# Optimization experiments

Measured on AMD Instinct MI355X. Metric: run time of the kernel, lower is better.

The kernel has to match this reference:

```python
import jax, jax.numpy as jnp
import numpy as np

B, S, D, H = 2, 2048, 1024, 16
HD = D // H


def setup_inputs() -> dict:
    key = jax.random.key(0)
    ks = jax.random.split(key, 7)
    mk = lambda k, shape, scale=1.0: (jax.random.normal(k, shape, dtype=jnp.float32) * scale)
    w_scale = 1.0 / np.sqrt(D)  # ~nn.Linear init scale
    return {
        "query": mk(ks[0], (B, S, D)),
        "key": mk(ks[1], (B, S, D)),
        "value": mk(ks[2], (B, S, D)),
        "Wq": mk(ks[3], (D, D), w_scale),
        "Wk": mk(ks[4], (D, D), w_scale),
        "Wv": mk(ks[5], (D, D), w_scale),
        "Wo": mk(ks[6], (D, D), w_scale),
    }


def reference(query, key, value, Wq, Wk, Wv, Wo):
    # torch nn.Linear(bias=False): y = x @ W.T, W is (out, in)
    def proj(x, W):
        y = jnp.einsum('bsd,ed->bse', x, W)          # [B, S, D]
        return y.reshape(x.shape[0], x.shape[1], H, HD).transpose(0, 2, 1, 3)  # [B, H, S, HD]

    Q = proj(query, Wq)
    K = proj(key, Wk)
    V = proj(value, Wv)

    # NOTE: original scales by sqrt(embedding_size), not sqrt(head_dim)
    scale = 1.0 / jnp.sqrt(jnp.asarray(D, dtype=Q.dtype))
    scores = jnp.einsum('bhqd,bhkd->bhqk', Q, K) * scale   # [B, H, Q, K]
    attn = jax.nn.softmax(scores, axis=-1)
    ctx = jnp.einsum('bhqk,bhkd->bhqd', attn, V)           # [B, H, Q, HD]
    ctx = ctx.transpose(0, 2, 1, 3).reshape(query.shape[0], query.shape[1], D)
    return jnp.einsum('bsd,ed->bse', ctx, Wo)
```

## Files before the change

kernel.cpp:

```cpp
#include <hip/hip_runtime.h>
#include <hip/hip_bf16.h>


typedef __bf16 bf16x8 __attribute__((ext_vector_type(8)));
typedef float f32x2 __attribute__((ext_vector_type(2)));
typedef float f32x4 __attribute__((ext_vector_type(4)));
typedef float f32x8 __attribute__((ext_vector_type(8)));
typedef float f32x16 __attribute__((ext_vector_type(16)));
typedef int i32x4 __attribute__((ext_vector_type(4)));

static constexpr int Bb = 2, Ss = 2048, Dd = 1024, Hh = 16, HDd = 64;
static constexpr int Mtot = Bb * Ss;

__global__ __launch_bounds__(256) void cast_all(
    const float* __restrict__ a0, const float* __restrict__ a1, const float* __restrict__ a2,
    const float* __restrict__ a3, const float* __restrict__ a4, const float* __restrict__ a5,
    const float* __restrict__ a6, __hip_bfloat16* __restrict__ d0, __hip_bfloat16* __restrict__ d1,
    __hip_bfloat16* __restrict__ d2, __hip_bfloat16* __restrict__ d3,
    __hip_bfloat16* __restrict__ d4, __hip_bfloat16* __restrict__ d5,
    __hip_bfloat16* __restrict__ d6, int nact8, int nw8) {
  const float* src;
  __hip_bfloat16* dst;
  int n8;
  switch (blockIdx.y) {
    case 0: src = a0; dst = d0; n8 = nact8; break;
    case 1: src = a1; dst = d1; n8 = nact8; break;
    case 2: src = a2; dst = d2; n8 = nact8; break;
    case 3: src = a3; dst = d3; n8 = nw8; break;
    case 4: src = a4; dst = d4; n8 = nw8; break;
    case 5: src = a5; dst = d5; n8 = nw8; break;
    default: src = a6; dst = d6; n8 = nw8; break;
  }
  int i = blockIdx.x * 256 + threadIdx.x;
  if (i >= n8) return;
  const float4* s4 = (const float4*)src + (size_t)i * 2;
  float4 a = s4[0], b = s4[1];
  union { __hip_bfloat16 h[8]; int4 v; } u;
  u.h[0] = __float2bfloat16(a.x); u.h[1] = __float2bfloat16(a.y);
  u.h[2] = __float2bfloat16(a.z); u.h[3] = __float2bfloat16(a.w);
  u.h[4] = __float2bfloat16(b.x); u.h[5] = __float2bfloat16(b.y);
  u.h[6] = __float2bfloat16(b.z); u.h[7] = __float2bfloat16(b.w);
  ((int4*)dst)[i] = u.v;
}

#define BM 128
#define BN 128
#define BK 64

__device__ __forceinline__ void gload_lds16(const void* g, void* l) {
  __builtin_amdgcn_global_load_lds((const __attribute__((address_space(1))) unsigned*)g,
                                   (__attribute__((address_space(3))) unsigned*)l, 16, 0, 0);
}

__device__ __forceinline__ void storeC(float* C, size_t idx, float v) { C[idx] = v; }
__device__ __forceinline__ void storeC(__hip_bfloat16* C, size_t idx, float v) {
  C[idx] = __float2bfloat16(v);
}

template <typename OutT>
__device__ __forceinline__ void gemm_bt_body(const __hip_bfloat16* __restrict__ A,
                                             const __hip_bfloat16* __restrict__ Bw,
                                             OutT* __restrict__ C, int K, int N) {
  __shared__ __hip_bfloat16 As[BM * BK];
  __shared__ __hip_bfloat16 Bs[BN * BK];
  const int tid = threadIdx.x;
  const int lane = tid & 63;
  const int wid = tid >> 6;
  const int wm = (wid >> 1) * 64;
  const int wn = (wid & 1) * 64;
  const int bm = blockIdx.x, bn = blockIdx.y;
  const int l15 = lane & 15;
  const int lhi = lane >> 4;

  f32x4 zero = {0.f, 0.f, 0.f, 0.f};
  f32x4 acc[4][4];
#pragma unroll
  for (int i = 0; i < 4; ++i)
#pragma unroll
    for (int j = 0; j < 4; ++j) acc[i][j] = zero;

  const size_t abase = (size_t)(bm * BM) * K;
  const size_t bbase = (size_t)(bn * BN) * K;

  for (int k0 = 0; k0 < K; k0 += BK) {
#pragma unroll
    for (int p = 0; p < 4; ++p) {
      int c = p * 256 + tid;
      int row = c >> 3;
      int col = (c & 7) * 8;
      gload_lds16(A + abase + (size_t)row * K + k0 + col, (char*)As + c * 16);
    }
#pragma unroll
    for (int p = 0; p < 4; ++p) {
      int c = p * 256 + tid;
      int row = c >> 3;
      int col = (c & 7) * 8;
      gload_lds16(Bw + bbase + (size_t)row * K + k0 + col, (char*)Bs + c * 16);
    }
    __syncthreads();
#pragma unroll
    for (int kk = 0; kk < 2; ++kk) {
      bf16x8 af[4], bfr[4];
#pragma unroll
      for (int mt = 0; mt < 4; ++mt)
        af[mt] = *(const bf16x8*)&As[(wm + mt * 16 + l15) * BK + kk * 32 + lhi * 8];
#pragma unroll
      for (int nt = 0; nt < 4; ++nt)
        bfr[nt] = *(const bf16x8*)&Bs[(wn + nt * 16 + l15) * BK + kk * 32 + lhi * 8];
#pragma unroll
      for (int mt = 0; mt < 4; ++mt)
#pragma unroll
        for (int nt = 0; nt < 4; ++nt)
          acc[mt][nt] = __builtin_amdgcn_mfma_f32_16x16x32_bf16(af[mt], bfr[nt], acc[mt][nt], 0, 0, 0);
    }
    __syncthreads();
  }

#pragma unroll
  for (int mt = 0; mt < 4; ++mt)
#pragma unroll
    for (int r = 0; r < 4; ++r) {
      int row = bm * BM + wm + mt * 16 + lhi * 4 + r;
#pragma unroll
      for (int nt = 0; nt < 4; ++nt) {
        int col = bn * BN + wn + nt * 16 + l15;
        storeC(C, (size_t)row * N + col, acc[mt][nt][r]);
      }
    }
}

__global__ __launch_bounds__(256) void qkv_proj(
    const __hip_bfloat16* __restrict__ xq, const __hip_bfloat16* __restrict__ xk,
    const __hip_bfloat16* __restrict__ xv, const __hip_bfloat16* __restrict__ wq,
    const __hip_bfloat16* __restrict__ wk, const __hip_bfloat16* __restrict__ wv,
    __hip_bfloat16* __restrict__ Qp, __hip_bfloat16* __restrict__ Kp,
    __hip_bfloat16* __restrict__ Vp) {
  const __hip_bfloat16* A;
  const __hip_bfloat16* W;
  __hip_bfloat16* C;
  if (blockIdx.z == 0) { A = xq; W = wq; C = Qp; }
  else if (blockIdx.z == 1) { A = xk; W = wk; C = Kp; }
  else { A = xv; W = wv; C = Vp; }
  gemm_bt_body<__hip_bfloat16>(A, W, C, Dd, Dd);
}

__global__ __launch_bounds__(256) void out_proj(const __hip_bfloat16* __restrict__ ctx,
                                                const __hip_bfloat16* __restrict__ wo,
                                                float* __restrict__ out) {
  gemm_bt_body<float>(ctx, wo, out, Dd, Dd);
}

__global__ __launch_bounds__(256) void transpose_v(const __hip_bfloat16* __restrict__ Vp,
                                                   __hip_bfloat16* __restrict__ Vt) {
  __shared__ __hip_bfloat16 T[64][72];
  const int tid = threadIdx.x;
  const int s0 = blockIdx.x * 64;
  const int bh = blockIdx.y;
  const int b = bh >> 4, h = bh & 15;
  const __hip_bfloat16* src = Vp + (size_t)b * Ss * Dd + (size_t)h * HDd;
#pragma unroll
  for (int p = 0; p < 2; ++p) {
    int id = p * 256 + tid;
    int r = id >> 3, c8 = (id & 7) * 8;
    *(int4*)&T[r][c8] = *(const int4*)(src + (size_t)(s0 + r) * Dd + c8);
  }
  __syncthreads();
#pragma unroll
  for (int p = 0; p < 2; ++p) {
    int id = p * 256 + tid;
    int d = id >> 3, s8 = (id & 7) * 8;
    union { int4 v; __hip_bfloat16 hh[8]; } u;
#pragma unroll
    for (int j = 0; j < 8; ++j) u.hh[j] = T[s8 + j][d];
    *(int4*)(Vt + ((size_t)bh * HDd + d) * Ss + s0 + s8) = u.v;
  }
}

__global__ __launch_bounds__(256) void attn_kernel(const __hip_bfloat16* __restrict__ Qp,
                                                   const __hip_bfloat16* __restrict__ Kp,
                                                   const __hip_bfloat16* __restrict__ Vt,
                                                   __hip_bfloat16* __restrict__ ctx) {
  constexpr int NT = Ss / 64;
  __shared__ __align__(16) __hip_bfloat16 Ks[3][64 * 64];
  __shared__ __align__(16) __hip_bfloat16 Vs[3][64 * 64];

  const int tid = threadIdx.x;
  const int lane = tid & 63, wid = tid >> 6;
  const int l31 = lane & 31;
  const bool hih = (lane >= 32);
  const int lhi2 = hih ? 1 : 0;

  const int bid = blockIdx.x;
  const int w = (bid & 7) * 64 + (bid >> 3);
  const int qblk = w & 15;
  const int bh = w >> 4;

  const int b = bh >> 4, h = bh & 15;
  const size_t head_off = (size_t)b * Ss * Dd + (size_t)h * HDd;
  const size_t vt_off = (size_t)bh * HDd * Ss;
  const int qrow = qblk * 128 + wid * 32 + l31;
  constexpr float scale = 0.03125f;
  constexpr float L2E = 1.44269504f;
  const float la = scale * L2E;

  bf16x8 qf[4];
#pragma unroll
  for (int ksd = 0; ksd < 4; ++ksd)
    qf[ksd] = *(const bf16x8*)(Qp + head_off + (size_t)qrow * Dd + ksd * 16 + lhi2 * 8);

  float l_run = 0.f;
  f32x16 o[2];
#pragma unroll
  for (int db = 0; db < 2; ++db)
#pragma unroll
    for (int r = 0; r < 16; ++r) o[db][r] = 0.f;

  auto stage = [&](int buf, int kv0) {
#pragma unroll
    for (int p = 0; p < 2; ++p) {
      int c = p * 256 + tid;
      int row = c >> 3;
      int sch = (c & 7) ^ (row & 7);
      gload_lds16(Kp + head_off + (size_t)(kv0 + row) * Dd + sch * 8,
                  (char*)&Ks[buf][0] + c * 16);
      gload_lds16(Vt + vt_off + (size_t)row * Ss + kv0 + sch * 8,
                  (char*)&Vs[buf][0] + c * 16);
    }
  };

  stage(0, 0);
  stage(1, 64);
  asm volatile("s_waitcnt vmcnt(4)" ::: "memory");
  __builtin_amdgcn_s_barrier();
  __builtin_amdgcn_sched_barrier(0);

  int cur = 0;
  for (int t = 0; t < NT; ++t) {
    int sbuf = cur + 2; if (sbuf >= 3) sbuf -= 3;
    if (t + 2 < NT) stage(sbuf, (t + 2) * 64);

    const char* kbase = (const char*)&Ks[cur][0];
    bf16x8 kfrag[2][4];
#pragma unroll
    for (int kb = 0; kb < 2; ++kb) {
      int row = kb * 32 + l31;
#pragma unroll
      for (int ksd = 0; ksd < 4; ++ksd)
        kfrag[kb][ksd] = *(const bf16x8*)(kbase + row * 128 +
                                          (((ksd * 2 + lhi2) ^ (row & 7)) << 4));
    }
    f32x16 st[2];
#pragma unroll
    for (int kb = 0; kb < 2; ++kb)
#pragma unroll
      for (int r = 0; r < 16; ++r) st[kb][r] = 0.f;
    __builtin_amdgcn_s_setprio(1);
#pragma unroll
    for (int kb = 0; kb < 2; ++kb)
#pragma unroll
      for (int ksd = 0; ksd < 4; ++ksd)
        st[kb] = __builtin_amdgcn_mfma_f32_32x32x16_bf16(kfrag[kb][ksd], qf[ksd], st[kb], 0, 0, 0);
    __builtin_amdgcn_s_setprio(0);

#pragma unroll
    for (int kb = 0; kb < 2; ++kb) {
      st[kb] = st[kb] * la;
#pragma unroll
      for (int r = 0; r < 16; ++r) st[kb][r] = exp2f(st[kb][r]);
    }

    f32x16 s16 = st[0] + st[1];
    f32x8 s8 = __builtin_shufflevector(s16, s16, 0, 1, 2, 3, 4, 5, 6, 7) +
               __builtin_shufflevector(s16, s16, 8, 9, 10, 11, 12, 13, 14, 15);
    f32x4 s4 = __builtin_shufflevector(s8, s8, 0, 1, 2, 3) +
               __builtin_shufflevector(s8, s8, 4, 5, 6, 7);
    f32x2 s2 = __builtin_shufflevector(s4, s4, 0, 1) + __builtin_shufflevector(s4, s4, 2, 3);
    float ps = s2[0] + s2[1];
    ps += __shfl_xor(ps, 32);
    l_run += ps;

    int cpk[2][4][2];
#pragma unroll
    for (int kb = 0; kb < 2; ++kb)
#pragma unroll
      for (int g = 0; g < 4; ++g)
#pragma unroll
        for (int i = 0; i < 2; ++i) {
          int rr;
          float lo = st[kb][g * 4 + 2 * i], hi = st[kb][g * 4 + 2 * i + 1];
          asm("v_cvt_pk_bf16_f32 %0, %1, %2" : "=v"(rr) : "v"(lo), "v"(hi));
          cpk[kb][g][i] = rr;
        }

    int own[2][2][2], rcv[2][2][2];
#pragma unroll
    for (int kb = 0; kb < 2; ++kb)
#pragma unroll
      for (int m = 0; m < 2; ++m)
#pragma unroll
        for (int i = 0; i < 2; ++i) {
          int cA = cpk[kb][2 * m][i];
          int cB = cpk[kb][2 * m + 1][i];
          int pay = hih ? cA : cB;
          own[kb][m][i] = hih ? cB : cA;
          rcv[kb][m][i] = __shfl_xor(pay, 32);
        }

    const char* vbase = (const char*)&Vs[cur][0];
    bf16x8 vfrag[4][2];
#pragma unroll
    for (int ks = 0; ks < 4; ++ks)
#pragma unroll
      for (int db = 0; db < 2; ++db) {
        int row = db * 32 + l31;
        vfrag[ks][db] = *(const bf16x8*)(vbase + row * 128 +
                                         (((ks * 2 + lhi2) ^ (row & 7)) << 4));
      }
    __builtin_amdgcn_s_setprio(1);
#pragma unroll
    for (int ks = 0; ks < 4; ++ks) {
      const int kb = ks >> 1, m = ks & 1;
      int w0 = hih ? rcv[kb][m][0] : own[kb][m][0];
      int w1 = hih ? rcv[kb][m][1] : own[kb][m][1];
      int w2 = hih ? own[kb][m][0] : rcv[kb][m][0];
      int w3 = hih ? own[kb][m][1] : rcv[kb][m][1];
      i32x4 bw = {w0, w1, w2, w3};
      bf16x8 pfrag = __builtin_bit_cast(bf16x8, bw);
#pragma unroll
      for (int db = 0; db < 2; ++db)
        o[db] = __builtin_amdgcn_mfma_f32_32x32x16_bf16(vfrag[ks][db], pfrag, o[db], 0, 0, 0);
    }
    __builtin_amdgcn_s_setprio(0);

    if (t + 1 < NT) {
      if (t + 2 < NT) {
        asm volatile("s_waitcnt vmcnt(4)" ::: "memory");
      } else {
        asm volatile("s_waitcnt vmcnt(0)" ::: "memory");
      }
      __builtin_amdgcn_s_barrier();
      __builtin_amdgcn_sched_barrier(0);
    }
    cur = (cur == 2) ? 0 : cur + 1;
  }

  float inv = 1.f / l_run;
  __hip_bfloat16* crow = ctx + head_off + (size_t)qrow * Dd;
#pragma unroll
  for (int db = 0; db < 2; ++db)
#pragma unroll
    for (int g = 0; g < 4; ++g) {
      union { uint2 v; __hip_bfloat16 hh[4]; } u;
#pragma unroll
      for (int a = 0; a < 4; ++a) u.hh[a] = __float2bfloat16(o[db][g * 4 + a] * inv);
      *(uint2*)(crow + db * 32 + 8 * g + 4 * lhi2) = u.v;
    }
}

extern "C" void kernel_launch(void* const* d_in, const int* in_sizes, int n_in,
                              void* d_out, int out_size, void* d_ws, size_t ws_size,
                              hipStream_t stream) {
  const float* q_f = (const float*)d_in[0];
  const float* k_f = (const float*)d_in[1];
  const float* v_f = (const float*)d_in[2];
  const float* wq_f = (const float*)d_in[3];
  const float* wk_f = (const float*)d_in[4];
  const float* wv_f = (const float*)d_in[5];
  const float* wo_f = (const float*)d_in[6];
  float* out = (float*)d_out;

  const size_t act = (size_t)Mtot * Dd;
  const size_t wsz = (size_t)Dd * Dd;
  char* ws = (char*)d_ws;
  __hip_bfloat16* qb = (__hip_bfloat16*)ws;   ws += act * 2;
  __hip_bfloat16* kb = (__hip_bfloat16*)ws;   ws += act * 2;
  __hip_bfloat16* vb = (__hip_bfloat16*)ws;   ws += act * 2;
  __hip_bfloat16* wqb = (__hip_bfloat16*)ws;  ws += wsz * 2;
  __hip_bfloat16* wkb = (__hip_bfloat16*)ws;  ws += wsz * 2;
  __hip_bfloat16* wvb = (__hip_bfloat16*)ws;  ws += wsz * 2;
  __hip_bfloat16* wob = (__hip_bfloat16*)ws;  ws += wsz * 2;
  __hip_bfloat16* Qp = (__hip_bfloat16*)ws;   ws += act * 2;
  __hip_bfloat16* Kp = (__hip_bfloat16*)ws;   ws += act * 2;
  __hip_bfloat16* Vp = (__hip_bfloat16*)ws;   ws += act * 2;
  __hip_bfloat16* Vt = (__hip_bfloat16*)ws;   ws += act * 2;
  __hip_bfloat16* ctxb = (__hip_bfloat16*)ws; ws += act * 2;

  dim3 gc((unsigned)(act / 8 / 256), 7);
  cast_all<<<gc, 256, 0, stream>>>(q_f, k_f, v_f, wq_f, wk_f, wv_f, wo_f, qb, kb, vb, wqb,
                                   wkb, wvb, wob, (int)(act / 8), (int)(wsz / 8));

  dim3 gq(Mtot / BM, Dd / BN, 3);
  qkv_proj<<<gq, 256, 0, stream>>>(qb, kb, vb, wqb, wkb, wvb, Qp, Kp, Vp);

  dim3 gt(Ss / 64, Bb * Hh);
  transpose_v<<<gt, 256, 0, stream>>>(Vp, Vt);

  attn_kernel<<<(Ss / 128) * (Bb * Hh), 256, 0, stream>>>(Qp, Kp, Vt, ctxb);

  dim3 go(Mtot / BM, Dd / BN);
  out_proj<<<go, 256, 0, stream>>>(ctxb, wob, out);
}
```

Baseline: 168.0 us.

## Split attention KV range in halves with merge kernel, fold softmax scale into Q

```diff
diff --git a/kernel.cpp b/kernel.cpp
--- a/kernel.cpp
+++ b/kernel.cpp
@@ -44,7 +44,6 @@
 }
 
 #define BM 128
-#define BN 128
 #define BK 64
 
 __device__ __forceinline__ void gload_lds16(const void* g, void* l) {
@@ -57,30 +56,31 @@
   C[idx] = __float2bfloat16(v);
 }
 
-template <typename OutT>
+template <typename OutT, int BNT>
 __device__ __forceinline__ void gemm_bt_body(const __hip_bfloat16* __restrict__ A,
                                              const __hip_bfloat16* __restrict__ Bw,
-                                             OutT* __restrict__ C, int K, int N) {
+                                             OutT* __restrict__ C, int K, int N, float cscale) {
+  constexpr int NTC = BNT / 32;
   __shared__ __hip_bfloat16 As[BM * BK];
-  __shared__ __hip_bfloat16 Bs[BN * BK];
+  __shared__ __hip_bfloat16 Bs[BNT * BK];
   const int tid = threadIdx.x;
   const int lane = tid & 63;
   const int wid = tid >> 6;
   const int wm = (wid >> 1) * 64;
-  const int wn = (wid & 1) * 64;
+  const int wn = (wid & 1) * (BNT / 2);
   const int bm = blockIdx.x, bn = blockIdx.y;
   const int l15 = lane & 15;
   const int lhi = lane >> 4;
 
   f32x4 zero = {0.f, 0.f, 0.f, 0.f};
-  f32x4 acc[4][4];
+  f32x4 acc[4][NTC];
 #pragma unroll
   for (int i = 0; i < 4; ++i)
 #pragma unroll
-    for (int j = 0; j < 4; ++j) acc[i][j] = zero;
+    for (int j = 0; j < NTC; ++j) acc[i][j] = zero;
 
   const size_t abase = (size_t)(bm * BM) * K;
-  const size_t bbase = (size_t)(bn * BN) * K;
+  const size_t bbase = (size_t)(bn * BNT) * K;
 
   for (int k0 = 0; k0 < K; k0 += BK) {
 #pragma unroll
@@ -91,7 +91,7 @@
       gload_lds16(A + abase + (size_t)row * K + k0 + col, (char*)As + c * 16);
     }
 #pragma unroll
-    for (int p = 0; p < 4; ++p) {
+    for (int p = 0; p < BNT / 32; ++p) {
       int c = p * 256 + tid;
       int row = c >> 3;
       int col = (c & 7) * 8;
@@ -100,17 +100,17 @@
     __syncthreads();
 #pragma unroll
     for (int kk = 0; kk < 2; ++kk) {
-      bf16x8 af[4], bfr[4];
+      bf16x8 af[4], bfr[NTC];
 #pragma unroll
       for (int mt = 0; mt < 4; ++mt)
         af[mt] = *(const bf16x8*)&As[(wm + mt * 16 + l15) * BK + kk * 32 + lhi * 8];
 #pragma unroll
-      for (int nt = 0; nt < 4; ++nt)
+      for (int nt = 0; nt < NTC; ++nt)
         bfr[nt] = *(const bf16x8*)&Bs[(wn + nt * 16 + l15) * BK + kk * 32 + lhi * 8];
 #pragma unroll
       for (int mt = 0; mt < 4; ++mt)
 #pragma unroll
-        for (int nt = 0; nt < 4; ++nt)
+        for (int nt = 0; nt < NTC; ++nt)
           acc[mt][nt] = __builtin_amdgcn_mfma_f32_16x16x32_bf16(af[mt], bfr[nt], acc[mt][nt], 0, 0, 0);
     }
     __syncthreads();
@@ -122,9 +122,9 @@
     for (int r = 0; r < 4; ++r) {
       int row = bm * BM + wm + mt * 16 + lhi * 4 + r;
 #pragma unroll
-      for (int nt = 0; nt < 4; ++nt) {
-        int col = bn * BN + wn + nt * 16 + l15;
-        storeC(C, (size_t)row * N + col, acc[mt][nt][r]);
+      for (int nt = 0; nt < NTC; ++nt) {
+        int col = bn * BNT + wn + nt * 16 + l15;
+        storeC(C, (size_t)row * N + col, acc[mt][nt][r] * cscale);
       }
     }
 }
@@ -138,16 +138,17 @@
   const __hip_bfloat16* A;
   const __hip_bfloat16* W;
   __hip_bfloat16* C;
-  if (blockIdx.z == 0) { A = xq; W = wq; C = Qp; }
+  float cs = 1.0f;
+  if (blockIdx.z == 0) { A = xq; W = wq; C = Qp; cs = 0.04508422f; }
   else if (blockIdx.z == 1) { A = xk; W = wk; C = Kp; }
   else { A = xv; W = wv; C = Vp; }
-  gemm_bt_body<__hip_bfloat16>(A, W, C, Dd, Dd);
+  gemm_bt_body<__hip_bfloat16, 128>(A, W, C, Dd, Dd, cs);
 }
 
 __global__ __launch_bounds__(256) void out_proj(const __hip_bfloat16* __restrict__ ctx,
                                                 const __hip_bfloat16* __restrict__ wo,
                                                 float* __restrict__ out) {
-  gemm_bt_body<float>(ctx, wo, out, Dd, Dd);
+  gemm_bt_body<float, 64>(ctx, wo, out, Dd, Dd, 1.0f);
 }
 
 __global__ __launch_bounds__(256) void transpose_v(const __hip_bfloat16* __restrict__ Vp,
@@ -179,8 +180,9 @@
 __global__ __launch_bounds__(256) void attn_kernel(const __hip_bfloat16* __restrict__ Qp,
                                                    const __hip_bfloat16* __restrict__ Kp,
                                                    const __hip_bfloat16* __restrict__ Vt,
-                                                   __hip_bfloat16* __restrict__ ctx) {
-  constexpr int NT = Ss / 64;
+                                                   float* __restrict__ Po,
+                                                   float* __restrict__ Pl) {
+  constexpr int HT = 16;
   __shared__ __align__(16) __hip_bfloat16 Ks[3][64 * 64];
   __shared__ __align__(16) __hip_bfloat16 Vs[3][64 * 64];
 
@@ -191,29 +193,31 @@
   const int lhi2 = hih ? 1 : 0;
 
   const int bid = blockIdx.x;
-  const int w = (bid & 7) * 64 + (bid >> 3);
-  const int qblk = w & 15;
-  const int bh = w >> 4;
+  const int w = (bid & 7) * 128 + (bid >> 3);
+  const int bh = w >> 5;
+  const int qblk = (w & 31) >> 1;
+  const int half = w & 1;
 
   const int b = bh >> 4, h = bh & 15;
   const size_t head_off = (size_t)b * Ss * Dd + (size_t)h * HDd;
   const size_t vt_off = (size_t)bh * HDd * Ss;
   const int qrow = qblk * 128 + wid * 32 + l31;
-  constexpr float scale = 0.03125f;
-  constexpr float L2E = 1.44269504f;
-  const float la = scale * L2E;
 
   bf16x8 qf[4];
 #pragma unroll
   for (int ksd = 0; ksd < 4; ++ksd)
     qf[ksd] = *(const bf16x8*)(Qp + head_off + (size_t)qrow * Dd + ksd * 16 + lhi2 * 8);
 
-  float l_run = 0.f;
-  f32x16 o[2];
+  const i32x4 onesbits = {0x3F803F80, 0x3F803F80, 0x3F803F80, 0x3F803F80};
+  const bf16x8 ones = __builtin_bit_cast(bf16x8, onesbits);
+
+  f32x16 o[2], ol;
 #pragma unroll
   for (int db = 0; db < 2; ++db)
 #pragma unroll
     for (int r = 0; r < 16; ++r) o[db][r] = 0.f;
+#pragma unroll
+  for (int r = 0; r < 16; ++r) ol[r] = 0.f;
 
   auto stage = [&](int buf, int kv0) {
 #pragma unroll
@@ -228,16 +232,17 @@
     }
   };
 
-  stage(0, 0);
-  stage(1, 64);
+  const int t0 = half * HT;
+  stage(0, (t0 + 0) * 64);
+  stage(1, (t0 + 1) * 64);
   asm volatile("s_waitcnt vmcnt(4)" ::: "memory");
   __builtin_amdgcn_s_barrier();
   __builtin_amdgcn_sched_barrier(0);
 
   int cur = 0;
-  for (int t = 0; t < NT; ++t) {
+  for (int t = 0; t < HT; ++t) {
     int sbuf = cur + 2; if (sbuf >= 3) sbuf -= 3;
-    if (t + 2 < NT) stage(sbuf, (t + 2) * 64);
+    if (t + 2 < HT) stage(sbuf, (t0 + t + 2) * 64);
 
     const char* kbase = (const char*)&Ks[cur][0];
     bf16x8 kfrag[2][4];
@@ -263,21 +268,9 @@
     __builtin_amdgcn_s_setprio(0);
 
 #pragma unroll
-    for (int kb = 0; kb < 2; ++kb) {
-      st[kb] = st[kb] * la;
+    for (int kb = 0; kb < 2; ++kb)
 #pragma unroll
       for (int r = 0; r < 16; ++r) st[kb][r] = exp2f(st[kb][r]);
-    }
-
-    f32x16 s16 = st[0] + st[1];
-    f32x8 s8 = __builtin_shufflevector(s16, s16, 0, 1, 2, 3, 4, 5, 6, 7) +
-               __builtin_shufflevector(s16, s16, 8, 9, 10, 11, 12, 13, 14, 15);
-    f32x4 s4 = __builtin_shufflevector(s8, s8, 0, 1, 2, 3) +
-               __builtin_shufflevector(s8, s8, 4, 5, 6, 7);
-    f32x2 s2 = __builtin_shufflevector(s4, s4, 0, 1) + __builtin_shufflevector(s4, s4, 2, 3);
-    float ps = s2[0] + s2[1];
-    ps += __shfl_xor(ps, 32);
-    l_run += ps;
 
     int cpk[2][4][2];
 #pragma unroll
@@ -329,11 +322,12 @@
 #pragma unroll
       for (int db = 0; db < 2; ++db)
         o[db] = __builtin_amdgcn_mfma_f32_32x32x16_bf16(vfrag[ks][db], pfrag, o[db], 0, 0, 0);
+      ol = __builtin_amdgcn_mfma_f32_32x32x16_bf16(ones, pfrag, ol, 0, 0, 0);
     }
     __builtin_amdgcn_s_setprio(0);
 
-    if (t + 1 < NT) {
-      if (t + 2 < NT) {
+    if (t + 1 < HT) {
+      if (t + 2 < HT) {
         asm volatile("s_waitcnt vmcnt(4)" ::: "memory");
       } else {
         asm volatile("s_waitcnt vmcnt(0)" ::: "memory");
@@ -344,17 +338,44 @@
     cur = (cur == 2) ? 0 : cur + 1;
   }
 
-  float inv = 1.f / l_run;
-  __hip_bfloat16* crow = ctx + head_off + (size_t)qrow * Dd;
+  const int qlocal = wid * 32 + l31;
+  float* prow = Po + (size_t)w * (128 * 64) + (size_t)qlocal * 64;
 #pragma unroll
   for (int db = 0; db < 2; ++db)
 #pragma unroll
     for (int g = 0; g < 4; ++g) {
-      union { uint2 v; __hip_bfloat16 hh[4]; } u;
-#pragma unroll
-      for (int a = 0; a < 4; ++a) u.hh[a] = __float2bfloat16(o[db][g * 4 + a] * inv);
-      *(uint2*)(crow + db * 32 + 8 * g + 4 * lhi2) = u.v;
-    }
+      f32x4 v4 = {o[db][g * 4 + 0], o[db][g * 4 + 1], o[db][g * 4 + 2], o[db][g * 4 + 3]};
+      *(f32x4*)(prow + db * 32 + 8 * g + 4 * lhi2) = v4;
+    }
+  if (!hih) Pl[(size_t)w * 128 + qlocal] = ol[0];
+}
+
+__global__ __launch_bounds__(256) void merge_halves(const float* __restrict__ Po,
+                                                    const float* __restrict__ Pl,
+                                                    __hip_bfloat16* __restrict__ ctx) {
+  const int mb = blockIdx.x;
+  const int bh = mb >> 4, qblk = mb & 15;
+  const int b = bh >> 4, h = bh & 15;
+  const int tid = threadIdx.x;
+  const int q = tid >> 1;
+  const int dh = (tid & 1) * 32;
+  const size_t w0 = (size_t)bh * 32 + qblk * 2;
+  const float* p0 = Po + w0 * (128 * 64) + (size_t)q * 64 + dh;
+  const float* p1 = p0 + 128 * 64;
+  float l = Pl[w0 * 128 + q] + Pl[w0 * 128 + 128 + q];
+  float inv = 1.f / l;
+  __hip_bfloat16* dst =
+      ctx + (size_t)b * Ss * Dd + (size_t)(qblk * 128 + q) * Dd + h * HDd + dh;
+#pragma unroll
+  for (int j = 0; j < 32; j += 4) {
+    f32x4 a = *(const f32x4*)(p0 + j);
+    f32x4 c = *(const f32x4*)(p1 + j);
+    f32x4 s = (a + c) * inv;
+    union { uint2 v; __hip_bfloat16 hh[4]; } u;
+#pragma unroll
+    for (int k = 0; k < 4; ++k) u.hh[k] = __float2bfloat16(s[k]);
+    *(uint2*)(dst + j) = u.v;
+  }
 }
 
 extern "C" void kernel_launch(void* const* d_in, const int* in_sizes, int n_in,
@@ -372,31 +393,39 @@
   const size_t act = (size_t)Mtot * Dd;
   const size_t wsz = (size_t)Dd * Dd;
   char* ws = (char*)d_ws;
-  __hip_bfloat16* qb = (__hip_bfloat16*)ws;   ws += act * 2;
-  __hip_bfloat16* kb = (__hip_bfloat16*)ws;   ws += act * 2;
-  __hip_bfloat16* vb = (__hip_bfloat16*)ws;   ws += act * 2;
-  __hip_bfloat16* wqb = (__hip_bfloat16*)ws;  ws += wsz * 2;
-  __hip_bfloat16* wkb = (__hip_bfloat16*)ws;  ws += wsz * 2;
-  __hip_bfloat16* wvb = (__hip_bfloat16*)ws;  ws += wsz * 2;
-  __hip_bfloat16* wob = (__hip_bfloat16*)ws;  ws += wsz * 2;
+
   __hip_bfloat16* Qp = (__hip_bfloat16*)ws;   ws += act * 2;
   __hip_bfloat16* Kp = (__hip_bfloat16*)ws;   ws += act * 2;
-  __hip_bfloat16* Vp = (__hip_bfloat16*)ws;   ws += act * 2;
   __hip_bfloat16* Vt = (__hip_bfloat16*)ws;   ws += act * 2;
   __hip_bfloat16* ctxb = (__hip_bfloat16*)ws; ws += act * 2;
+  __hip_bfloat16* wob = (__hip_bfloat16*)ws;  ws += wsz * 2;
+
+  char* scratch = ws;
+  __hip_bfloat16* qb = (__hip_bfloat16*)scratch;
+  __hip_bfloat16* kb = qb + act;
+  __hip_bfloat16* vb = kb + act;
+  __hip_bfloat16* wqb = vb + act;
+  __hip_bfloat16* wkb = wqb + wsz;
+  __hip_bfloat16* wvb = wkb + wsz;
+  __hip_bfloat16* Vp = wvb + wsz;
+
+  float* Po = (float*)scratch;
+  float* Pl = Po + (size_t)1024 * 128 * 64;
 
   dim3 gc((unsigned)(act / 8 / 256), 7);
   cast_all<<<gc, 256, 0, stream>>>(q_f, k_f, v_f, wq_f, wk_f, wv_f, wo_f, qb, kb, vb, wqb,
                                    wkb, wvb, wob, (int)(act / 8), (int)(wsz / 8));
 
-  dim3 gq(Mtot / BM, Dd / BN, 3);
+  dim3 gq(Mtot / BM, Dd / 128, 3);
   qkv_proj<<<gq, 256, 0, stream>>>(qb, kb, vb, wqb, wkb, wvb, Qp, Kp, Vp);
 
   dim3 gt(Ss / 64, Bb * Hh);
   transpose_v<<<gt, 256, 0, stream>>>(Vp, Vt);
 
-  attn_kernel<<<(Ss / 128) * (Bb * Hh), 256, 0, stream>>>(Qp, Kp, Vt, ctxb);
-
-  dim3 go(Mtot / BM, Dd / BN);
+  attn_kernel<<<1024, 256, 0, stream>>>(Qp, Kp, Vt, Po, Pl);
+
+  merge_halves<<<512, 256, 0, stream>>>(Po, Pl, ctxb);
+
+  dim3 go(Mtot / BM, Dd / 64);
   out_proj<<<go, 256, 0, stream>>>(ctxb, wob, out);
 }
```

Result: slower. 173.3 us (+3.1%).
